# Performance work log

Hardware: AMD Instinct MI355X
Metric: run time of the kernel (lower is better)

The kernel has to match this reference:

```python
import jax, jax.numpy as jnp
import numpy as np

NUM_HEADS = 8
DIM_HEAD = 64
GROUPS = 32
EPS = 1e-5


def setup_inputs() -> dict:
    key = jax.random.key(0)
    k1, k2, k3 = jax.random.split(key, 3)
    C = 512
    inner = NUM_HEADS * DIM_HEAD  # 512
    x = jax.random.normal(k1, (8, C, 32, 32), dtype=jnp.float32)
    gamma = jnp.ones((C,), dtype=jnp.float32)
    beta = jnp.zeros((C,), dtype=jnp.float32)
    w_qkv = jax.random.normal(k2, (3 * inner, C), dtype=jnp.float32) * 0.02
    w_out = jax.random.normal(k3, (C, inner), dtype=jnp.float32) * 0.02
    return {"x": x, "gamma": gamma, "beta": beta, "w_qkv": w_qkv, "w_out": w_out}


def group_norm(x, gamma, beta):
    b, c, h, w = x.shape
    xg = x.reshape(b, GROUPS, c // GROUPS, h, w)
    mean = jnp.mean(xg, axis=(2, 3, 4), keepdims=True)
    var = jnp.var(xg, axis=(2, 3, 4), keepdims=True)
    xn = ((xg - mean) * jax.lax.rsqrt(var + EPS)).reshape(b, c, h, w)
    return xn * gamma[None, :, None, None] + beta[None, :, None, None]


def reference(x, gamma, beta, w_qkv, w_out):
    b, c, h, w = x.shape
    H, d = NUM_HEADS, DIM_HEAD
    inner = H * d
    scale = d ** (-0.5)
    residual = x
    xn = group_norm(x, gamma, beta)
    # 1x1 conv (no bias) == channel matmul
    qkv = jnp.einsum('bchw,oc->bohw', xn, w_qkv)  # [b, 3*inner, h, w]
    q, k, v = jnp.split(qkv, 3, axis=1)
    def to_heads(t):
        # b (H d) h w -> b H (h w) d
        return t.reshape(b, H, d, h * w).transpose(0, 1, 3, 2)
    q, k, v = to_heads(q), to_heads(k), to_heads(v)
    attn = jnp.einsum('bhid,bhjd->bhij', q, k) * scale  # [b,H,hw,hw]
    attn = jax.nn.softmax(attn, axis=-1)
    out = jnp.einsum('bhij,bhjd->bhid', attn, v)  # [b,H,hw,d]
    # b H (h w) d -> b (H d) h w
    out = out.transpose(0, 1, 3, 2).reshape(b, inner, h, w)
    out = jnp.einsum('bchw,oc->bohw', out, w_out)
    return out + residual
```

## Files before the change

### kernel.cpp

```cpp
#include <hip/hip_runtime.h>


typedef __attribute__((ext_vector_type(8))) short bf16x8;
typedef __attribute__((ext_vector_type(4))) short bf16x4;
typedef __attribute__((ext_vector_type(4))) float f32x4;

#define NB 8
#define NC 512
#define HW 1024
#define NHEAD 8
#define DHEAD 64
#define GROUPS 32
#define CPG 16
#define QKV_N 1536

#define GLL16(gaddr, ldsaddr)                                                  \
    __builtin_amdgcn_global_load_lds(                                          \
        (const __attribute__((address_space(1))) unsigned*)(gaddr),            \
        (__attribute__((address_space(3))) unsigned*)(ldsaddr), 16, 0, 0)

__device__ alignas(64) short g_xn[(size_t)8192 * 512];
__device__ alignas(64) short g_qkv[(size_t)8192 * 1536];
__device__ alignas(64) short g_vt[(size_t)64 * 64 * 1024];
__device__ alignas(64) short g_attno[(size_t)8192 * 512];
__device__ alignas(64) short g_wqkv[(size_t)1536 * 512];
__device__ alignas(64) short g_wout[(size_t)512 * 512];

__device__ __forceinline__ float b2f(short h) {
    union { unsigned u; float f; } v;
    v.u = ((unsigned)(unsigned short)h) << 16;
    return v.f;
}
__device__ __forceinline__ short f2b(float f) {
    union { float f; unsigned u; } v;
    v.f = f;
    unsigned r = v.u + 0x7fff + ((v.u >> 16) & 1);
    return (short)(r >> 16);
}

__global__ __launch_bounds__(256) void conv_weights(
    const float* __restrict__ wqkv, const float* __restrict__ wout) {
    int i = blockIdx.x * 256 + threadIdx.x;
    if (i < 1536 * 512) {
        float v = wqkv[i];
        if (i < 512 * 512) v *= 0.125f;
        g_wqkv[i] = f2b(v);
    }
    if (i < 512 * 512)  g_wout[i] = f2b(wout[i]);
}

__global__ __launch_bounds__(256) void gn_kernel(
    const float* __restrict__ x, const float* __restrict__ gamma,
    const float* __restrict__ beta) {
    int b = blockIdx.x >> 5, g = blockIdx.x & 31;
    int tid = threadIdx.x;
    __shared__ alignas(16) short tile[CPG][HW];
    __shared__ float red[2][4];
    __shared__ float sg[CPG], sb[CPG];
    if (tid < CPG) {
        int cg = g * CPG + tid;
        sg[tid] = gamma[cg];
        sb[tid] = beta[cg];
    }
    const float* xb = x + (size_t)b * NC * HW + (size_t)g * CPG * HW;
    float s1 = 0.f, s2 = 0.f;
    #pragma unroll
    for (int it = 0; it < 8; it++) {
        int idx = tid + it * 256;
        f32x4 v0 = *(const f32x4*)(xb + idx * 8);
        f32x4 v1 = *(const f32x4*)(xb + idx * 8 + 4);
        bf16x8 w;
        #pragma unroll
        for (int j = 0; j < 4; j++) {
            s1 += v0[j] + v1[j]; s2 += v0[j] * v0[j] + v1[j] * v1[j];
            w[j] = f2b(v0[j]); w[j + 4] = f2b(v1[j]);
        }
        *(bf16x8*)(&((short*)tile)[idx * 8]) = w;
    }
    #pragma unroll
    for (int off = 32; off; off >>= 1) { s1 += __shfl_xor(s1, off); s2 += __shfl_xor(s2, off); }
    int wid = tid >> 6;
    if ((tid & 63) == 0) { red[0][wid] = s1; red[1][wid] = s2; }
    __syncthreads();
    float t1 = red[0][0] + red[0][1] + red[0][2] + red[0][3];
    float t2 = red[1][0] + red[1][1] + red[1][2] + red[1][3];
    float mean = t1 * (1.f / 16384.f);
    float var  = t2 * (1.f / 16384.f) - mean * mean;
    float inv  = rsqrtf(var + 1e-5f);
    #pragma unroll
    for (int p = 0; p < 4; p++) {
        int s = tid * 4 + p;
        bf16x8 pk0, pk1;
        #pragma unroll
        for (int cc = 0; cc < 8; cc++) {
            pk0[cc] = f2b((b2f(tile[cc][s])     - mean) * inv * sg[cc]     + sb[cc]);
            pk1[cc] = f2b((b2f(tile[cc + 8][s]) - mean) * inv * sg[cc + 8] + sb[cc + 8]);
        }
        size_t dst = ((size_t)(b * HW + s)) * NC + g * CPG;
        *(bf16x8*)(g_xn + dst)     = pk0;
        *(bf16x8*)(g_xn + dst + 8) = pk1;
    }
}

__global__ __launch_bounds__(256) void gemm_qkv() {
    const int K = NC;
    int tid = threadIdx.x, lane = tid & 63, wid = tid >> 6;
    int quad = lane >> 4, l15 = lane & 15;
    int row0 = blockIdx.x * 128;
    int col0 = blockIdx.y * 128;
    __shared__ alignas(16) short sa[128 * 32];
    __shared__ alignas(16) short sbuf[128 * 32];
    int srow = wid * 32 + (lane >> 2);
    int scol = (lane & 3) * 8;
    const short* ga = g_xn   + (size_t)(row0 + srow) * K + scol;
    const short* gb = g_wqkv + (size_t)(col0 + srow) * K + scol;
    short* la = sa   + wid * 1024;
    short* lb = sbuf + wid * 1024;
    int mw = (wid >> 1) * 64, nw = (wid & 1) * 64;
    f32x4 acc[4][4] = {};
    for (int k = 0; k < K; k += 32) {
        GLL16(ga + k, la);
        GLL16(ga + (size_t)16 * K + k, la + 512);
        GLL16(gb + k, lb);
        GLL16(gb + (size_t)16 * K + k, lb + 512);
        __syncthreads();
        bf16x8 af[4], bfv[4];
        #pragma unroll
        for (int m = 0; m < 4; m++) af[m]  = *(const bf16x8*)&sa[(mw + m * 16 + l15) * 32 + quad * 8];
        #pragma unroll
        for (int n = 0; n < 4; n++) bfv[n] = *(const bf16x8*)&sbuf[(nw + n * 16 + l15) * 32 + quad * 8];
        #pragma unroll
        for (int m = 0; m < 4; m++)
            #pragma unroll
            for (int n = 0; n < 4; n++)
                acc[m][n] = __builtin_amdgcn_mfma_f32_16x16x32_bf16(af[m], bfv[n], acc[m][n], 0, 0, 0);
        __syncthreads();
    }
    #pragma unroll
    for (int m = 0; m < 4; m++)
        #pragma unroll
        for (int n = 0; n < 4; n++)
            #pragma unroll
            for (int r = 0; r < 4; r++) {
                int row = row0 + mw + m * 16 + quad * 4 + r;
                int col = col0 + nw + n * 16 + l15;
                g_qkv[(size_t)row * QKV_N + col] = f2b(acc[m][n][r]);
            }
}

__global__ __launch_bounds__(256) void transpose_v() {
    int bh = blockIdx.x & 63, st = blockIdx.x >> 6;
    int b = bh >> 3, h = bh & 7;
    int tid = threadIdx.x;
    __shared__ alignas(16) short tile[64][72];
    int s0 = st * 64;
    #pragma unroll
    for (int cc = 0; cc < 2; cc++) {
        int idx = tid + cc * 256;
        int s = idx >> 3, dc = idx & 7;
        *(bf16x8*)&tile[s][dc * 8] =
            *(const bf16x8*)(g_qkv + ((size_t)(b * HW + s0 + s)) * QKV_N + 1024 + h * DHEAD + dc * 8);
    }
    __syncthreads();
    #pragma unroll
    for (int cc = 0; cc < 2; cc++) {
        int idx = tid + cc * 256;
        int d = idx & 63, sc = idx >> 6;
        bf16x8 o;
        #pragma unroll
        for (int j = 0; j < 8; j++) o[j] = tile[sc * 8 + j][d];
        *(bf16x8*)(g_vt + ((size_t)(bh * 64 + d)) * HW + s0 + sc * 8) = o;
    }
}

__global__ __launch_bounds__(256) void attn_kernel() {
    int bh = blockIdx.x & 63, qt = blockIdx.x >> 6;
    int b = bh >> 3, h = bh & 7;
    int tid = threadIdx.x, lane = tid & 63, wid = tid >> 6;
    int quad = lane >> 4, l15 = lane & 15;
    __shared__ alignas(16) short kt[2][64 * 64];
    __shared__ alignas(16) short vt[2][64 * 64];
    __shared__ alignas(16) short pt[4][64][36];
    int qrow0 = qt * 128 + wid * 32;

    bf16x8 aq[2][2];
    #pragma unroll
    for (int mi = 0; mi < 2; mi++) {
        const short* qb = g_qkv + ((size_t)(b * HW + qrow0 + mi * 16 + l15)) * QKV_N + h * DHEAD + quad * 8;
        aq[mi][0] = *(const bf16x8*)qb;
        aq[mi][1] = *(const bf16x8*)(qb + 32);
    }
    f32x4 acc_o[2][4] = {};
    float l_part[2][4] = {};

    int r_lo = lane >> 3;
    int s_log = (lane & 7) ^ r_lo;
    int swz = l15 & 7;

    auto stage = [&](int it, int bufi) {
        int t0 = it * 64;
        #pragma unroll
        for (int c = 0; c < 2; c++) {
            int r = wid * 16 + c * 8 + r_lo;
            GLL16(g_qkv + ((size_t)(b * HW + t0 + r)) * QKV_N + 512 + h * DHEAD + s_log * 8,
                  &kt[bufi][(wid * 16 + c * 8) * 64]);
            GLL16(g_vt + ((size_t)(bh * 64 + r)) * HW + t0 + s_log * 8,
                  &vt[bufi][(wid * 16 + c * 8) * 64]);
        }
    };

    stage(0, 0);
    __syncthreads();
    for (int it = 0; it < 16; it++) {
        int cur = it & 1;
        if (it < 15) stage(it + 1, cur ^ 1);
        f32x4 sv[2][4];
        #pragma unroll
        for (int sub = 0; sub < 4; sub++) {
            int row = sub * 16 + l15;
            bf16x8 b0 = *(const bf16x8*)&kt[cur][row * 64 + ((quad ^ swz) * 8)];
            bf16x8 b1 = *(const bf16x8*)&kt[cur][row * 64 + (((4 + quad) ^ swz) * 8)];
            #pragma unroll
            for (int mi = 0; mi < 2; mi++) {
                f32x4 z = {};
                z = __builtin_amdgcn_mfma_f32_16x16x32_bf16(aq[mi][0], b0, z, 0, 0, 0);
                z = __builtin_amdgcn_mfma_f32_16x16x32_bf16(aq[mi][1], b1, z, 0, 0, 0);
                sv[mi][sub] = z;
            }
        }
        #pragma unroll
        for (int mi = 0; mi < 2; mi++)
            #pragma unroll
            for (int sub = 0; sub < 4; sub++) {
                unsigned u[4];
                #pragma unroll
                for (int r = 0; r < 4; r++) {
                    float e = __expf(sv[mi][sub][r]);
                    l_part[mi][r] += e;
                    union { float f; unsigned b; } cv; cv.f = e;
                    u[r] = cv.b + 0x8000u;
                }
                unsigned d0 = (u[0] >> 16) | (u[1] & 0xffff0000u);
                unsigned d1 = (u[2] >> 16) | (u[3] & 0xffff0000u);
                union { unsigned w[2]; bf16x4 s; } pk;
                pk.w[0] = d0; pk.w[1] = d1;
                *(bf16x4*)&pt[wid][sub * 16 + l15][mi * 16 + quad * 4] = pk.s;
            }
        asm volatile("" ::: "memory");
        bf16x8 ap[2][2];
        #pragma unroll
        for (int mi = 0; mi < 2; mi++)
            #pragma unroll
            for (int j = 0; j < 8; j++) {
                ap[mi][0][j] = pt[wid][quad * 8 + j][mi * 16 + l15];
                ap[mi][1][j] = pt[wid][32 + quad * 8 + j][mi * 16 + l15];
            }
        #pragma unroll
        for (int nd = 0; nd < 4; nd++) {
            int row = nd * 16 + l15;
            bf16x8 bv0 = *(const bf16x8*)&vt[cur][row * 64 + ((quad ^ swz) * 8)];
            bf16x8 bv1 = *(const bf16x8*)&vt[cur][row * 64 + (((4 + quad) ^ swz) * 8)];
            #pragma unroll
            for (int mi = 0; mi < 2; mi++) {
                acc_o[mi][nd] = __builtin_amdgcn_mfma_f32_16x16x32_bf16(ap[mi][0], bv0, acc_o[mi][nd], 0, 0, 0);
                acc_o[mi][nd] = __builtin_amdgcn_mfma_f32_16x16x32_bf16(ap[mi][1], bv1, acc_o[mi][nd], 0, 0, 0);
            }
        }
        __syncthreads();
    }
    #pragma unroll
    for (int mi = 0; mi < 2; mi++)
        #pragma unroll
        for (int r = 0; r < 4; r++) {
            float l = l_part[mi][r];
            l += __shfl_xor(l, 1); l += __shfl_xor(l, 2);
            l += __shfl_xor(l, 4); l += __shfl_xor(l, 8);
            float invl = 1.f / l;
            size_t row = (size_t)(b * HW + qrow0 + mi * 16 + quad * 4 + r);
            #pragma unroll
            for (int nd = 0; nd < 4; nd++)
                g_attno[row * NC + h * DHEAD + nd * 16 + l15] = f2b(acc_o[mi][nd][r] * invl);
        }
}

__global__ __launch_bounds__(256) void gemm_out(
    const float* __restrict__ xres, float* __restrict__ out) {
    const int K = NC;
    int tid = threadIdx.x, lane = tid & 63, wid = tid >> 6;
    int quad = lane >> 4, l15 = lane & 15;
    int row0 = blockIdx.x * 128;
    int col0 = blockIdx.y * 128;
    __shared__ alignas(16) short sa[128 * 32];
    __shared__ alignas(16) short sbuf[128 * 32];
    int srow = wid * 32 + (lane >> 2);
    int scol = (lane & 3) * 8;
    const short* ga = g_wout  + (size_t)(row0 + srow) * K + scol;
    const short* gb = g_attno + (size_t)(col0 + srow) * K + scol;
    short* la = sa   + wid * 1024;
    short* lb = sbuf + wid * 1024;
    int mw = (wid >> 1) * 64, nw = (wid & 1) * 64;
    f32x4 acc[4][4] = {};
    for (int k = 0; k < K; k += 32) {
        GLL16(ga + k, la);
        GLL16(ga + (size_t)16 * K + k, la + 512);
        GLL16(gb + k, lb);
        GLL16(gb + (size_t)16 * K + k, lb + 512);
        __syncthreads();
        bf16x8 af[4], bfv[4];
        #pragma unroll
        for (int m = 0; m < 4; m++) af[m]  = *(const bf16x8*)&sa[(mw + m * 16 + l15) * 32 + quad * 8];
        #pragma unroll
        for (int n = 0; n < 4; n++) bfv[n] = *(const bf16x8*)&sbuf[(nw + n * 16 + l15) * 32 + quad * 8];
        #pragma unroll
        for (int m = 0; m < 4; m++)
            #pragma unroll
            for (int n = 0; n < 4; n++)
                acc[m][n] = __builtin_amdgcn_mfma_f32_16x16x32_bf16(af[m], bfv[n], acc[m][n], 0, 0, 0);
        __syncthreads();
    }
    #pragma unroll
    for (int m = 0; m < 4; m++)
        #pragma unroll
        for (int n = 0; n < 4; n++)
            #pragma unroll
            for (int r = 0; r < 4; r++) {
                int o  = row0 + mw + m * 16 + quad * 4 + r;
                int bs = col0 + nw + n * 16 + l15;
                size_t addr = (size_t)(bs >> 10) * ((size_t)NC * HW) + (size_t)o * HW + (bs & 1023);
                out[addr] = acc[m][n][r] + xres[addr];
            }
}

extern "C" void kernel_launch(void* const* d_in, const int* in_sizes, int n_in,
                              void* d_out, int out_size, void* d_ws, size_t ws_size,
                              hipStream_t stream) {
    const float* x     = (const float*)d_in[0];
    const float* gamma = (const float*)d_in[1];
    const float* beta  = (const float*)d_in[2];
    const float* wqkv  = (const float*)d_in[3];
    const float* wout  = (const float*)d_in[4];
    float* out = (float*)d_out;

    conv_weights<<<dim3(3072), dim3(256), 0, stream>>>(wqkv, wout);
    gn_kernel<<<dim3(NB * GROUPS), dim3(256), 0, stream>>>(x, gamma, beta);
    gemm_qkv<<<dim3(64, 12), dim3(256), 0, stream>>>();
    transpose_v<<<dim3(1024), dim3(256), 0, stream>>>();
    attn_kernel<<<dim3(512), dim3(256), 0, stream>>>();
    gemm_out<<<dim3(4, 64), dim3(256), 0, stream>>>(x, out);
}
```

Baseline: 157.1 us.

## Fuse weight conversion into groupnorm kernel and transpose QK^T MFMA in attention

Merges the weight bf16 conversion kernel into the groupnorm kernel as 64 extra grid-stride blocks, which removes one launch and lets both jobs run concurrently. In attention, the QK^T MFMA operands are swapped to produce S^T. Each lane then holds four consecutive key columns of one query row, so P can be stored and reloaded with packed 4-element LDS accesses instead of 8 scalar gathers per fragment. The row-sum reduction moves from per-lane shuffles to a shuffle over quads plus a broadcast. The catch is the longer strided loop in the 64 conversion blocks, which may now lengthen the prep kernel's tail.

New measurement: 158.3 us. About the same (+0.8%).

```diff
diff --git a/kernel.cpp b/kernel.cpp
--- a/kernel.cpp
+++ b/kernel.cpp
@@ -38,22 +38,23 @@
     return (short)(r >> 16);
 }
 
-__global__ __launch_bounds__(256) void conv_weights(
-    const float* __restrict__ wqkv, const float* __restrict__ wout) {
-    int i = blockIdx.x * 256 + threadIdx.x;
-    if (i < 1536 * 512) {
-        float v = wqkv[i];
-        if (i < 512 * 512) v *= 0.125f;
-        g_wqkv[i] = f2b(v);
-    }
-    if (i < 512 * 512)  g_wout[i] = f2b(wout[i]);
-}
-
-__global__ __launch_bounds__(256) void gn_kernel(
+__global__ __launch_bounds__(256) void prep_kernel(
     const float* __restrict__ x, const float* __restrict__ gamma,
-    const float* __restrict__ beta) {
+    const float* __restrict__ beta, const float* __restrict__ wqkv,
+    const float* __restrict__ wout) {
+    int tid = threadIdx.x;
+    if (blockIdx.x >= 256) {
+        int wb = blockIdx.x - 256;
+        for (int i = wb * 256 + tid; i < 1536 * 512; i += 64 * 256) {
+            float v = wqkv[i];
+            if (i < 512 * 512) v *= 0.125f;
+            g_wqkv[i] = f2b(v);
+        }
+        for (int i = wb * 256 + tid; i < 512 * 512; i += 64 * 256)
+            g_wout[i] = f2b(wout[i]);
+        return;
+    }
     int b = blockIdx.x >> 5, g = blockIdx.x & 31;
-    int tid = threadIdx.x;
     __shared__ alignas(16) short tile[CPG][HW];
     __shared__ float red[2][4];
     __shared__ float sg[CPG], sb[CPG];
@@ -180,18 +181,18 @@
     int quad = lane >> 4, l15 = lane & 15;
     __shared__ alignas(16) short kt[2][64 * 64];
     __shared__ alignas(16) short vt[2][64 * 64];
-    __shared__ alignas(16) short pt[4][64][36];
+    __shared__ alignas(16) short pt4[4][16][32][4];
     int qrow0 = qt * 128 + wid * 32;
 
     bf16x8 aq[2][2];
     #pragma unroll
-    for (int mi = 0; mi < 2; mi++) {
-        const short* qb = g_qkv + ((size_t)(b * HW + qrow0 + mi * 16 + l15)) * QKV_N + h * DHEAD + quad * 8;
-        aq[mi][0] = *(const bf16x8*)qb;
-        aq[mi][1] = *(const bf16x8*)(qb + 32);
+    for (int mt = 0; mt < 2; mt++) {
+        const short* qb = g_qkv + ((size_t)(b * HW + qrow0 + mt * 16 + l15)) * QKV_N + h * DHEAD + quad * 8;
+        aq[mt][0] = *(const bf16x8*)qb;
+        aq[mt][1] = *(const bf16x8*)(qb + 32);
     }
     f32x4 acc_o[2][4] = {};
-    float l_part[2][4] = {};
+    float l_part[2] = {0.f, 0.f};
 
     int r_lo = lane >> 3;
     int s_log = (lane & 7) ^ r_lo;
@@ -214,46 +215,47 @@
     for (int it = 0; it < 16; it++) {
         int cur = it & 1;
         if (it < 15) stage(it + 1, cur ^ 1);
-        f32x4 sv[2][4];
+        f32x4 st[4][2];
         #pragma unroll
         for (int sub = 0; sub < 4; sub++) {
             int row = sub * 16 + l15;
-            bf16x8 b0 = *(const bf16x8*)&kt[cur][row * 64 + ((quad ^ swz) * 8)];
-            bf16x8 b1 = *(const bf16x8*)&kt[cur][row * 64 + (((4 + quad) ^ swz) * 8)];
-            #pragma unroll
-            for (int mi = 0; mi < 2; mi++) {
+            bf16x8 k0 = *(const bf16x8*)&kt[cur][row * 64 + ((quad ^ swz) * 8)];
+            bf16x8 k1 = *(const bf16x8*)&kt[cur][row * 64 + (((4 + quad) ^ swz) * 8)];
+            #pragma unroll
+            for (int mt = 0; mt < 2; mt++) {
                 f32x4 z = {};
-                z = __builtin_amdgcn_mfma_f32_16x16x32_bf16(aq[mi][0], b0, z, 0, 0, 0);
-                z = __builtin_amdgcn_mfma_f32_16x16x32_bf16(aq[mi][1], b1, z, 0, 0, 0);
-                sv[mi][sub] = z;
-            }
-        }
-        #pragma unroll
-        for (int mi = 0; mi < 2; mi++)
-            #pragma unroll
-            for (int sub = 0; sub < 4; sub++) {
+                z = __builtin_amdgcn_mfma_f32_16x16x32_bf16(k0, aq[mt][0], z, 0, 0, 0);
+                z = __builtin_amdgcn_mfma_f32_16x16x32_bf16(k1, aq[mt][1], z, 0, 0, 0);
+                st[sub][mt] = z;
+            }
+        }
+        #pragma unroll
+        for (int sub = 0; sub < 4; sub++)
+            #pragma unroll
+            for (int mt = 0; mt < 2; mt++) {
                 unsigned u[4];
                 #pragma unroll
                 for (int r = 0; r < 4; r++) {
-                    float e = __expf(sv[mi][sub][r]);
-                    l_part[mi][r] += e;
+                    float e = __expf(st[sub][mt][r]);
+                    l_part[mt] += e;
                     union { float f; unsigned b; } cv; cv.f = e;
                     u[r] = cv.b + 0x8000u;
                 }
-                unsigned d0 = (u[0] >> 16) | (u[1] & 0xffff0000u);
-                unsigned d1 = (u[2] >> 16) | (u[3] & 0xffff0000u);
                 union { unsigned w[2]; bf16x4 s; } pk;
-                pk.w[0] = d0; pk.w[1] = d1;
-                *(bf16x4*)&pt[wid][sub * 16 + l15][mi * 16 + quad * 4] = pk.s;
+                pk.w[0] = (u[0] >> 16) | (u[1] & 0xffff0000u);
+                pk.w[1] = (u[2] >> 16) | (u[3] & 0xffff0000u);
+                *(bf16x4*)&pt4[wid][sub * 4 + quad][mt * 16 + l15][0] = pk.s;
             }
         asm volatile("" ::: "memory");
         bf16x8 ap[2][2];
         #pragma unroll
         for (int mi = 0; mi < 2; mi++)
             #pragma unroll
-            for (int j = 0; j < 8; j++) {
-                ap[mi][0][j] = pt[wid][quad * 8 + j][mi * 16 + l15];
-                ap[mi][1][j] = pt[wid][32 + quad * 8 + j][mi * 16 + l15];
+            for (int half = 0; half < 2; half++) {
+                union { bf16x4 h[2]; bf16x8 v; } cc;
+                cc.h[0] = *(const bf16x4*)&pt4[wid][half * 8 + quad * 2][mi * 16 + l15][0];
+                cc.h[1] = *(const bf16x4*)&pt4[wid][half * 8 + quad * 2 + 1][mi * 16 + l15][0];
+                ap[mi][half] = cc.v;
             }
         #pragma unroll
         for (int nd = 0; nd < 4; nd++) {
@@ -269,18 +271,19 @@
         __syncthreads();
     }
     #pragma unroll
-    for (int mi = 0; mi < 2; mi++)
+    for (int mi = 0; mi < 2; mi++) {
+        float lf = l_part[mi];
+        lf += __shfl_xor(lf, 16); lf += __shfl_xor(lf, 32);
         #pragma unroll
         for (int r = 0; r < 4; r++) {
-            float l = l_part[mi][r];
-            l += __shfl_xor(l, 1); l += __shfl_xor(l, 2);
-            l += __shfl_xor(l, 4); l += __shfl_xor(l, 8);
-            float invl = 1.f / l;
+            float lr = __shfl(lf, quad * 4 + r);
+            float invl = 1.f / lr;
             size_t row = (size_t)(b * HW + qrow0 + mi * 16 + quad * 4 + r);
             #pragma unroll
             for (int nd = 0; nd < 4; nd++)
                 g_attno[row * NC + h * DHEAD + nd * 16 + l15] = f2b(acc_o[mi][nd][r] * invl);
         }
+    }
 }
 
 __global__ __launch_bounds__(256) void gemm_out(
@@ -341,8 +344,7 @@
     const float* wout  = (const float*)d_in[4];
     float* out = (float*)d_out;
 
-    conv_weights<<<dim3(3072), dim3(256), 0, stream>>>(wqkv, wout);
-    gn_kernel<<<dim3(NB * GROUPS), dim3(256), 0, stream>>>(x, gamma, beta);
+    prep_kernel<<<dim3(320), dim3(256), 0, stream>>>(x, gamma, beta, wqkv, wout);
     gemm_qkv<<<dim3(64, 12), dim3(256), 0, stream>>>();
     transpose_v<<<dim3(1024), dim3(256), 0, stream>>>();
     attn_kernel<<<dim3(512), dim3(256), 0, stream>>>();
```
